# Performance work log

Measured on AMD Instinct MI355X. Metric: run time of the kernel, lower is better.

The kernel has to match this reference:

```python
import jax, jax.numpy as jnp
import numpy as np

ALPHA = 0.2  # LeakyReLU negative slope
N, F_IN, F_OUT = 8192, 512, 64
NEG_INF = -9e15


def setup_inputs() -> dict:
    key = jax.random.key(0)
    k1, k2, k3, k4 = jax.random.split(key, 4)
    inp = jax.random.normal(k1, (N, F_IN), dtype=jnp.float32)
    adj = jax.random.randint(k2, (N, N), 0, 2, dtype=jnp.int32)
    W = jax.random.normal(k3, (F_IN, F_OUT), dtype=jnp.float32) * (1.414 / np.sqrt(F_IN))
    a = jax.random.normal(k4, (2 * F_OUT, 1), dtype=jnp.float32) * 0.1
    return {"input": inp, "adj": adj, "W": W, "a": a, "sparse": 0}


def reference(input, adj, W, a, sparse):
    h = input @ W  # [N, F_out]
    # Decompose concat([h_i, h_j]) @ a into additive src/dst terms (same math,
    # avoids the O(N^2 * 2F) intermediate): e_ij = leakyrelu(h_i@a1 + h_j@a2)
    f_src = h @ a[:F_OUT]   # [N, 1]
    f_dst = h @ a[F_OUT:]   # [N, 1]
    e = jax.nn.leaky_relu(f_src + f_dst.T, ALPHA)  # [N, N]
    attention = jnp.where(adj > 0, e, NEG_INF)
    attention = jax.nn.softmax(attention, axis=1)
    h_prime = attention @ h  # [N, F_out]
    return jax.nn.leaky_relu(h_prime, 0.01)[None]  # concat=True path; default F.leaky_relu slope 0.01
```

## Files before the change

kernel.cpp:

```cpp
#include <hip/hip_runtime.h>
#include <hip/hip_bf16.h>

#define N 8192
#define FIN 512
#define FOUT 64
#define ALPHA 0.2f

typedef __bf16 bf16x8 __attribute__((ext_vector_type(8)));
typedef __bf16 bf16x4 __attribute__((ext_vector_type(4)));
typedef float f32x4 __attribute__((ext_vector_type(4)));
typedef int i32x4 __attribute__((ext_vector_type(4)));


__device__ __forceinline__ unsigned enc_f(float x) {
    unsigned u = __float_as_uint(x);
    return (u & 0x80000000u) ? ~u : (u | 0x80000000u);
}
__device__ __forceinline__ float dec_f(unsigned u) {
    return (u & 0x80000000u) ? __uint_as_float(u & 0x7FFFFFFFu) : __uint_as_float(~u);
}

__global__ __launch_bounds__(64) void k_wt(const float* __restrict__ W,
                                           __bf16* __restrict__ WtG) {
    const int g = blockIdx.x * 64 + threadIdx.x;
    const int k = g >> 3;
    const int f0 = (g & 7) * 8;
    const float4 w0 = *(const float4*)(W + (size_t)k * FOUT + f0);
    const float4 w1 = *(const float4*)(W + (size_t)k * FOUT + f0 + 4);
    WtG[(size_t)(f0 + 0) * FIN + k] = (__bf16)w0.x;
    WtG[(size_t)(f0 + 1) * FIN + k] = (__bf16)w0.y;
    WtG[(size_t)(f0 + 2) * FIN + k] = (__bf16)w0.z;
    WtG[(size_t)(f0 + 3) * FIN + k] = (__bf16)w0.w;
    WtG[(size_t)(f0 + 4) * FIN + k] = (__bf16)w1.x;
    WtG[(size_t)(f0 + 5) * FIN + k] = (__bf16)w1.y;
    WtG[(size_t)(f0 + 6) * FIN + k] = (__bf16)w1.z;
    WtG[(size_t)(f0 + 7) * FIN + k] = (__bf16)w1.w;
}

__global__ __launch_bounds__(64) void k12(const float* __restrict__ in,
                                          const __bf16* __restrict__ WtG,
                                          const float* __restrict__ a,
                                          float* __restrict__ f_src,
                                          float* __restrict__ f_dst,
                                          unsigned* __restrict__ Mkey,
                                          __bf16* __restrict__ hT) {
    __shared__ __bf16 tb[64][16];
    const int lane = threadIdx.x;
    const int m = lane & 15, quad = lane >> 4;
    const int i0 = blockIdx.x * 16;

    f32x4 acc[4];
#pragma unroll
    for (int t = 0; t < 4; ++t) acc[t] = (f32x4){0.f, 0.f, 0.f, 0.f};

    const float* arow = in + (size_t)(i0 + m) * FIN + quad * 8;
    for (int k0 = 0; k0 < FIN; k0 += 32) {
        const float4 x0 = *(const float4*)(arow + k0);
        const float4 x1 = *(const float4*)(arow + k0 + 4);
        bf16x8 af;
        af[0] = (__bf16)x0.x; af[1] = (__bf16)x0.y; af[2] = (__bf16)x0.z; af[3] = (__bf16)x0.w;
        af[4] = (__bf16)x1.x; af[5] = (__bf16)x1.y; af[6] = (__bf16)x1.z; af[7] = (__bf16)x1.w;
#pragma unroll
        for (int t = 0; t < 4; ++t) {
            const bf16x8 bf = *(const bf16x8*)(WtG + (size_t)(t * 16 + m) * FIN + k0 + quad * 8);
            acc[t] = __builtin_amdgcn_mfma_f32_16x16x32_bf16(af, bf, acc[t], 0, 0, 0);
        }
    }
    float s1[4], s2[4];
#pragma unroll
    for (int r = 0; r < 4; ++r) { s1[r] = 0.f; s2[r] = 0.f; }
#pragma unroll
    for (int t = 0; t < 4; ++t) {
        const float a1 = a[t * 16 + m], a2 = a[64 + t * 16 + m];
#pragma unroll
        for (int r = 0; r < 4; ++r) {
            s1[r] += acc[t][r] * a1;
            s2[r] += acc[t][r] * a2;
        }
    }
#pragma unroll
    for (int off = 1; off <= 8; off <<= 1)
#pragma unroll
        for (int r = 0; r < 4; ++r) {
            s1[r] += __shfl_xor(s1[r], off);
            s2[r] += __shfl_xor(s2[r], off);
        }
    float lm = -1e30f;
    if (m == 0) {
#pragma unroll
        for (int r = 0; r < 4; ++r) {
            f_src[i0 + quad * 4 + r] = s1[r];
            f_dst[i0 + quad * 4 + r] = s2[r];
            lm = fmaxf(lm, s2[r]);
        }
    }
    lm = fmaxf(lm, __shfl_xor(lm, 16));
    lm = fmaxf(lm, __shfl_xor(lm, 32));
    if (lane == 0) atomicMax(Mkey, enc_f(lm));

#pragma unroll
    for (int t = 0; t < 4; ++t)
#pragma unroll
        for (int r = 0; r < 4; ++r) tb[t * 16 + m][quad * 4 + r] = (__bf16)acc[t][r];
    __syncthreads();
    {
        const int f = lane;
        const bf16x8 v0 = *(const bf16x8*)&tb[f][0];
        const bf16x8 v1 = *(const bf16x8*)&tb[f][8];
        *(bf16x8*)(hT + (size_t)f * N + i0) = v0;
        *(bf16x8*)(hT + (size_t)f * N + i0 + 8) = v1;
    }
}

__global__ __launch_bounds__(256, 4) void k3_attn(const int* __restrict__ adj,
                                                  const float* __restrict__ f_src,
                                                  const float* __restrict__ fdstG,
                                                  const unsigned* __restrict__ Mkey,
                                                  const __bf16* __restrict__ hT,
                                                  float* __restrict__ num,
                                                  float* __restrict__ lsum) {
    __shared__ float sfd[1024];
    __shared__ __bf16 wl[4][16][256];
    const int tid = threadIdx.x;
    const int wv = tid >> 6, lane = tid & 63;
    const int m = lane & 15, quad = lane >> 4;
    const int i0 = __builtin_amdgcn_readfirstlane(blockIdx.x * 64 + wv * 16);
    const int jb = blockIdx.y * 1024;
    const float LOG2E = 1.44269504088896f;

    *(f32x4*)&sfd[tid * 4] = *(const f32x4*)(fdstG + jb + tid * 4);
    __syncthreads();

    const float M = dec_f(*Mkey);
    float fsr[16], shl[16];
#pragma unroll
    for (int r = 0; r < 16; ++r) {
        const float fs = f_src[i0 + r];
        const float t0 = fs + M;
        fsr[r] = fs;
        shl[r] = fmaxf(t0, ALPHA * t0) * LOG2E;
    }

    f32x4 acc[4];
#pragma unroll
    for (int t = 0; t < 4; ++t) acc[t] = (f32x4){0.f, 0.f, 0.f, 0.f};
    f32x4 accl = (f32x4){0.f, 0.f, 0.f, 0.f};

    bf16x8 bones;
#pragma unroll
    for (int jj = 0; jj < 8; ++jj) bones[jj] = (__bf16)(m == 0 ? 1.0f : 0.0f);

    const int* ap = adj + (size_t)i0 * N + jb + lane * 4;

    for (int jt = 0; jt < 1024; jt += 256) {
        i32x4 adjv[16];
#pragma unroll
        for (int r = 0; r < 16; ++r)
            adjv[r] = __builtin_nontemporal_load((const i32x4*)(ap + (size_t)r * N + jt));

        const f32x4 fd = *(const f32x4*)&sfd[jt + lane * 4];

#pragma unroll
        for (int r = 0; r < 16; ++r) {
            bf16x4 wb;
#pragma unroll
            for (int c = 0; c < 4; ++c) {
                float e = fsr[r] + fd[c];
                e = fmaxf(e, ALPHA * e);
                const float ex = __builtin_amdgcn_exp2f(e * LOG2E - shl[r]);
                wb[c] = (__bf16)(adjv[r][c] > 0 ? ex : 0.f);
            }
            *(bf16x4*)&wl[wv][r][(lane * 4) ^ ((r & 7) << 3)] = wb;
        }

#pragma unroll
        for (int jj0 = 0; jj0 < 256; jj0 += 64) {
#pragma unroll
            for (int u = 0; u < 2; ++u) {
                const int cb = jj0 + u * 32 + quad * 8;
                const bf16x8 af = *(const bf16x8*)&wl[wv][m][cb ^ ((m & 7) << 3)];
#pragma unroll
                for (int t = 0; t < 4; ++t) {
                    const bf16x8 bfr =
                        *(const bf16x8*)(hT + (size_t)(t * 16 + m) * N + jb + jt + cb);
                    acc[t] = __builtin_amdgcn_mfma_f32_16x16x32_bf16(af, bfr, acc[t], 0, 0, 0);
                }
                accl = __builtin_amdgcn_mfma_f32_16x16x32_bf16(af, bones, accl, 0, 0, 0);
            }
        }
    }
#pragma unroll
    for (int t = 0; t < 4; ++t)
#pragma unroll
        for (int r = 0; r < 4; ++r)
            atomicAdd(&num[(size_t)(i0 + quad * 4 + r) * FOUT + t * 16 + m], acc[t][r]);
    if (m == 0) {
#pragma unroll
        for (int r = 0; r < 4; ++r) atomicAdd(&lsum[i0 + quad * 4 + r], accl[r]);
    }
}

__global__ __launch_bounds__(256) void k4_norm(float* __restrict__ out,
                                               const float* __restrict__ lsum) {
    const int idx = blockIdx.x * 256 + threadIdx.x;
    const float l = lsum[idx >> 6];
    const float v = out[idx] / (l > 0.f ? l : 1.f);
    out[idx] = v > 0.f ? v : 0.01f * v;
}

extern "C" void kernel_launch(void* const* d_in, const int* in_sizes, int n_in,
                              void* d_out, int out_size, void* d_ws, size_t ws_size,
                              hipStream_t stream) {
    const float* in = (const float*)d_in[0];
    const int* adj = (const int*)d_in[1];
    const float* W = (const float*)d_in[2];
    const float* a = (const float*)d_in[3];
    float* out = (float*)d_out;

    char* ws = (char*)d_ws;
    unsigned* Mkey = (unsigned*)ws;
    float* lsum = (float*)(ws + 64);
    float* f_src = (float*)(ws + 32832);
    float* f_dst = (float*)(ws + 65600);
    __bf16* WtG = (__bf16*)(ws + 98368);
    __bf16* hT = (__bf16*)(ws + 163904);

    hipMemsetAsync(ws, 0, 64 + N * 4, stream);
    hipMemsetAsync(d_out, 0, (size_t)N * FOUT * sizeof(float), stream);

    k_wt<<<64, 64, 0, stream>>>(W, WtG);
    k12<<<N / 16, 64, 0, stream>>>(in, WtG, a, f_src, f_dst, Mkey, hT);

    dim3 g3(N / 64, 8);
    k3_attn<<<g3, 256, 0, stream>>>(adj, f_src, f_dst, Mkey, hT, out, lsum);
    k4_norm<<<(N * FOUT) / 256, 256, 0, stream>>>(out, lsum);
}
```

Baseline: 449.9 us.

## Stage hT tile in shared memory and shrink attention j-tile to 128

The attention kernel now loads each 64x128 slice of hT cooperatively into LDS once per block, so the four waves read it from shared memory instead of each re-reading it from global memory. The j-tile shrinks from 256 to 128 and the adjacency load is remapped so each lane covers alternating rows with a 128-column stride. This cuts redundant global/L2 traffic for hT and reduces per-thread adjacency registers. In exchange it adds two block-wide barriers per tile and doubles the number of tile iterations.

New measurement: 397.3 us. 1.13x faster.

```diff
diff --git a/kernel.cpp b/kernel.cpp
--- a/kernel.cpp
+++ b/kernel.cpp
@@ -112,6 +112,8 @@
     }
 }
 
+constexpr int JT = 128;
+
 __global__ __launch_bounds__(256, 4) void k3_attn(const int* __restrict__ adj,
                                                   const float* __restrict__ f_src,
                                                   const float* __restrict__ fdstG,
@@ -119,17 +121,19 @@
                                                   const __bf16* __restrict__ hT,
                                                   float* __restrict__ num,
                                                   float* __restrict__ lsum) {
+    __shared__ __bf16 sh[64][JT + 8];
+    __shared__ __bf16 wl[4][16][JT];
     __shared__ float sfd[1024];
-    __shared__ __bf16 wl[4][16][256];
     const int tid = threadIdx.x;
     const int wv = tid >> 6, lane = tid & 63;
     const int m = lane & 15, quad = lane >> 4;
-    const int i0 = __builtin_amdgcn_readfirstlane(blockIdx.x * 64 + wv * 16);
+    const int rpar = lane >> 5;
+    const int col4 = (lane & 31) * 4;
+    const int i0 = blockIdx.x * 64 + wv * 16;
     const int jb = blockIdx.y * 1024;
     const float LOG2E = 1.44269504088896f;
 
     *(f32x4*)&sfd[tid * 4] = *(const f32x4*)(fdstG + jb + tid * 4);
-    __syncthreads();
 
     const float M = dec_f(*Mkey);
     float fsr[16], shl[16];
@@ -150,39 +154,50 @@
 #pragma unroll
     for (int jj = 0; jj < 8; ++jj) bones[jj] = (__bf16)(m == 0 ? 1.0f : 0.0f);
 
-    const int* ap = adj + (size_t)i0 * N + jb + lane * 4;
-
-    for (int jt = 0; jt < 1024; jt += 256) {
-        i32x4 adjv[16];
-#pragma unroll
-        for (int r = 0; r < 16; ++r)
-            adjv[r] = __builtin_nontemporal_load((const i32x4*)(ap + (size_t)r * N + jt));
-
-        const f32x4 fd = *(const f32x4*)&sfd[jt + lane * 4];
-
-#pragma unroll
-        for (int r = 0; r < 16; ++r) {
+    const int* apL = adj + (size_t)(i0 + rpar) * N + jb + col4;
+
+    for (int jt = 0; jt < 1024; jt += JT) {
+        __syncthreads();
+
+        i32x4 adjv[8];
+#pragma unroll
+        for (int v = 0; v < 8; ++v)
+            adjv[v] = __builtin_nontemporal_load((const i32x4*)(apL + (size_t)(2 * v) * N + jt));
+
+#pragma unroll
+        for (int it = 0; it < 4; ++it) {
+            const int c = tid + it * 256;
+            const int f = c >> 4, off = (c & 15) * 8;
+            *(bf16x8*)&sh[f][off] = *(const bf16x8*)(hT + (size_t)f * N + jb + jt + off);
+        }
+        __syncthreads();
+
+        const f32x4 fd = *(const f32x4*)&sfd[jt + col4];
+#pragma unroll
+        for (int v = 0; v < 8; ++v) {
+            const float fs_l = rpar ? fsr[2 * v + 1] : fsr[2 * v];
+            const float sh_l = rpar ? shl[2 * v + 1] : shl[2 * v];
+            const int rr = 2 * v + rpar;
             bf16x4 wb;
 #pragma unroll
             for (int c = 0; c < 4; ++c) {
-                float e = fsr[r] + fd[c];
+                float e = fs_l + fd[c];
                 e = fmaxf(e, ALPHA * e);
-                const float ex = __builtin_amdgcn_exp2f(e * LOG2E - shl[r]);
-                wb[c] = (__bf16)(adjv[r][c] > 0 ? ex : 0.f);
+                const float ex = __builtin_amdgcn_exp2f(e * LOG2E - sh_l);
+                wb[c] = (__bf16)(adjv[v][c] > 0 ? ex : 0.f);
             }
-            *(bf16x4*)&wl[wv][r][(lane * 4) ^ ((r & 7) << 3)] = wb;
-        }
-
-#pragma unroll
-        for (int jj0 = 0; jj0 < 256; jj0 += 64) {
+            *(bf16x4*)&wl[wv][rr][col4 ^ ((rr & 7) << 3)] = wb;
+        }
+
+#pragma unroll
+        for (int jj0 = 0; jj0 < JT; jj0 += 64) {
 #pragma unroll
             for (int u = 0; u < 2; ++u) {
                 const int cb = jj0 + u * 32 + quad * 8;
                 const bf16x8 af = *(const bf16x8*)&wl[wv][m][cb ^ ((m & 7) << 3)];
 #pragma unroll
                 for (int t = 0; t < 4; ++t) {
-                    const bf16x8 bfr =
-                        *(const bf16x8*)(hT + (size_t)(t * 16 + m) * N + jb + jt + cb);
+                    const bf16x8 bfr = *(const bf16x8*)&sh[t * 16 + m][cb];
                     acc[t] = __builtin_amdgcn_mfma_f32_16x16x32_bf16(af, bfr, acc[t], 0, 0, 0);
                 }
                 accl = __builtin_amdgcn_mfma_f32_16x16x32_bf16(af, bones, accl, 0, 0, 0);
```
